# Kernel optimization log

Hardware: AMD Instinct MI355X
Metric: run time of the kernel (lower is better)

The kernel has to match this reference:

```python
import jax, jax.numpy as jnp
import numpy as np

TOP_K = 8
ROUTED_SCALING_FACTOR = 2.5
NORM_TOPK_PROB = True


def setup_inputs() -> dict:
    key = jax.random.key(0)
    k1, k2 = jax.random.split(key)
    hidden_states = jax.random.normal(k1, (4, 4096, 4096), dtype=jnp.float32)
    # gate weight: (n_routed_experts, hidden_size)
    weight = jax.random.normal(k2, (256, 4096), dtype=jnp.float32) * (1.0 / np.sqrt(4096))
    return {"hidden_states": hidden_states, "weight": weight}


def reference(hidden_states, weight):
    bsz, seq_len, h = hidden_states.shape
    x = hidden_states.reshape(-1, h).astype(jnp.float32)  # [T, h]
    # gate logits: [T, E]
    logits = jnp.einsum("th,eh->te", x, weight.astype(jnp.float32))
    scores = jax.nn.softmax(logits, axis=-1)
    topk_weight, topk_idx = jax.lax.top_k(scores, TOP_K)  # [T, k]
    if TOP_K > 1 and NORM_TOPK_PROB:
        denom = jnp.sum(topk_weight, axis=-1, keepdims=True) + 1e-20
        topk_weight = topk_weight / denom * ROUTED_SCALING_FACTOR
    else:
        topk_weight = topk_weight * ROUTED_SCALING_FACTOR
    return (topk_idx, topk_weight)
```

## Files before the change

kernel.cpp:

```cpp
#include <hip/hip_runtime.h>
#include <math.h>

typedef _Float16 half8  __attribute__((ext_vector_type(8)));
typedef _Float16 half4v __attribute__((ext_vector_type(4)));
typedef float    f32x16 __attribute__((ext_vector_type(16)));

namespace {
constexpr int H      = 4096;
constexpr int E      = 256;
constexpr int TOPK   = 8;
constexpr int NCAND  = 12;
constexpr int BM     = 64;
constexpr int BK     = 32;
constexpr int NCHUNK = H / BK;
constexpr int SLD    = E + 4;
constexpr float DELTA = 5e-4f;
constexpr size_t WF_BYTES = (size_t)E * H * 2 * 2;
constexpr int SMEM_BYTES = BM * SLD * 4;
}

__global__ void convert_w_kernel(const float* __restrict__ W,
                                 _Float16* __restrict__ Wf) {
    int t  = blockIdx.x * blockDim.x + threadIdx.x;
    int e  = t >> 10;
    int kq = t & 1023;
    float4 w4 = *(const float4*)(W + ((size_t)e << 12) + (kq << 2));
    float x0 = w4.x * 64.0f, x1 = w4.y * 64.0f, x2 = w4.z * 64.0f, x3 = w4.w * 64.0f;
    _Float16 h0 = (_Float16)x0, h1 = (_Float16)x1, h2 = (_Float16)x2, h3 = (_Float16)x3;
    _Float16 l0 = (_Float16)(x0 - (float)h0), l1 = (_Float16)(x1 - (float)h1);
    _Float16 l2 = (_Float16)(x2 - (float)h2), l3 = (_Float16)(x3 - (float)h3);
    int k    = kq << 2;
    int nt   = e >> 5;
    int ks   = k >> 4;
    int lane = (e & 31) | (((k >> 3) & 1) << 5);
    int j    = k & 7;
    size_t base = (((size_t)nt * 256 + ks) * 2) * 512 + lane * 8 + j;
    half4v hv = {h0, h1, h2, h3};
    half4v lv = {l0, l1, l2, l3};
    *(half4v*)(Wf + base)       = hv;
    *(half4v*)(Wf + base + 512) = lv;
}

struct BF { half8 h[2][2]; half8 l[2][2]; };

__global__ __launch_bounds__(512, 2)
void moe_gate_mfma(const float* __restrict__ X, const _Float16* __restrict__ Wf,
                   const float* __restrict__ Wg,
                   float* __restrict__ out_idx, float* __restrict__ out_w) {
    __shared__ __align__(16) char smem[SMEM_BYTES];
    _Float16* Abuf = (_Float16*)smem;
    float*    sc   = (float*)smem;

    const int tid  = threadIdx.x;
    const int lane = tid & 63;
    const int wave = tid >> 6;
    const int wr   = wave >> 2;
    const int wc   = wave & 3;
    const int m0   = blockIdx.x * BM;

    const int m_s  = tid >> 3;
    const int kq_s = tid & 7;
    const int ks_s = kq_s >> 2;
    const int mt_s = m_s >> 5;
    const int ln_s = (m_s & 31) | (((kq_s >> 1) & 1) << 5);
    const int j_s  = (kq_s & 1) * 4;
    const int dst_s = ((ks_s * 2 + mt_s) * 2) * 512 + ln_s * 8 + j_s;
    const float* xgp = X + (size_t)(m0 + m_s) * H + kq_s * 4;

    f32x16 acc[2];
    #pragma unroll
    for (int nt = 0; nt < 2; ++nt)
        #pragma unroll
        for (int r = 0; r < 16; ++r) acc[nt][r] = 0.0f;

    auto load_b = [&](int kc, BF& b) {
        #pragma unroll
        for (int ks = 0; ks < 2; ++ks)
            #pragma unroll
            for (int nt = 0; nt < 2; ++nt) {
                size_t base = (((size_t)(2 * wc + nt) * 256 + (kc * 2 + ks)) * 2) * 512
                              + lane * 8;
                b.h[ks][nt] = *(const half8*)(Wf + base);
                b.l[ks][nt] = *(const half8*)(Wf + base + 512);
            }
    };
    auto stage = [&](int bufIdx, float4 xv) {
        _Float16* buf = Abuf + bufIdx * 4096;
        float x0 = xv.x, x1 = xv.y, x2 = xv.z, x3 = xv.w;
        _Float16 h0 = (_Float16)x0, h1 = (_Float16)x1, h2 = (_Float16)x2, h3 = (_Float16)x3;
        _Float16 l0 = (_Float16)(x0 - (float)h0), l1 = (_Float16)(x1 - (float)h1);
        _Float16 l2 = (_Float16)(x2 - (float)h2), l3 = (_Float16)(x3 - (float)h3);
        half4v hv = {h0, h1, h2, h3};
        half4v lv = {l0, l1, l2, l3};
        *(half4v*)(buf + dst_s)       = hv;
        *(half4v*)(buf + dst_s + 512) = lv;
    };
    auto compute = [&](int bufIdx, const BF& b) {
        const _Float16* buf = Abuf + bufIdx * 4096;
        #pragma unroll
        for (int ks = 0; ks < 2; ++ks) {
            const _Float16* p = buf + (ks * 2 + wr) * 1024 + lane * 8;
            half8 a_hi = *(const half8*)p;
            half8 a_lo = *(const half8*)(p + 512);
            #pragma unroll
            for (int nt = 0; nt < 2; ++nt) {
                acc[nt] = __builtin_amdgcn_mfma_f32_32x32x16_f16(a_hi, b.h[ks][nt], acc[nt], 0, 0, 0);
                acc[nt] = __builtin_amdgcn_mfma_f32_32x32x16_f16(a_lo, b.h[ks][nt], acc[nt], 0, 0, 0);
                acc[nt] = __builtin_amdgcn_mfma_f32_32x32x16_f16(a_hi, b.l[ks][nt], acc[nt], 0, 0, 0);
            }
        }
    };

    BF bcur;
    load_b(0, bcur);
    float4 xv = *(const float4*)(xgp);
    stage(0, xv);
    __syncthreads();
    float4 xnxt = *(const float4*)(xgp + BK);

    for (int kc = 0; kc < NCHUNK; ++kc) {
        BF bnxt;
        float4 xfar = make_float4(0.f, 0.f, 0.f, 0.f);
        if (kc + 1 < NCHUNK) load_b(kc + 1, bnxt);
        if (kc + 2 < NCHUNK) xfar = *(const float4*)(xgp + (size_t)(kc + 2) * BK);
        compute(kc & 1, bcur);
        if (kc + 1 < NCHUNK) {
            stage((kc + 1) & 1, xnxt);
            __syncthreads();
        }
        bcur = bnxt;
        xnxt = xfar;
    }

    __syncthreads();
    #pragma unroll
    for (int nt = 0; nt < 2; ++nt) {
        #pragma unroll
        for (int r = 0; r < 16; ++r) {
            int row = (r & 3) + 8 * (r >> 2) + 4 * (lane >> 5);
            int col = lane & 31;
            sc[(wr * 32 + row) * SLD + wc * 64 + nt * 32 + col] = acc[nt][r] * 0.015625f;
        }
    }
    __syncthreads();

    for (int t8 = 0; t8 < 8; ++t8) {
        const int t = wave * 8 + t8;
        float4 pv = *(const float4*)(sc + t * SLD + lane * 4);
        float p0 = pv.x, p1 = pv.y, p2 = pv.z, p3 = pv.w;

        float tv[NCAND]; int ti[NCAND];
        #pragma unroll
        for (int s = 0; s < NCAND; ++s) {
            float bv = p0; int bi = lane * 4;
            if (p1 > bv || (p1 == bv && lane * 4 + 1 < bi)) { bv = p1; bi = lane * 4 + 1; }
            if (p2 > bv || (p2 == bv && lane * 4 + 2 < bi)) { bv = p2; bi = lane * 4 + 2; }
            if (p3 > bv || (p3 == bv && lane * 4 + 3 < bi)) { bv = p3; bi = lane * 4 + 3; }
            #pragma unroll
            for (int off = 32; off > 0; off >>= 1) {
                float ov = __shfl_xor(bv, off, 64);
                int   oi = __shfl_xor(bi, off, 64);
                if (ov > bv || (ov == bv && oi < bi)) { bv = ov; bi = oi; }
            }
            tv[s] = bv; ti[s] = bi;
            if ((bi >> 2) == lane) {
                const int sl = bi & 3;
                if      (sl == 0) p0 = -3e38f;
                else if (sl == 1) p1 = -3e38f;
                else if (sl == 2) p2 = -3e38f;
                else              p3 = -3e38f;
            }
        }

        bool rescue = false;
        #pragma unroll
        for (int g = 0; g < 9; ++g) rescue |= (tv[g] - tv[g + 1] < DELTA);

        if (rescue) {
            double dv[NCAND];
            const float* xr = X + (size_t)(m0 + t) * H;
            #pragma unroll 1
            for (int c = 0; c < NCAND; ++c) {
                const float* wrow = Wg + (size_t)ti[c] * H;
                double s_ = 0.0;
                #pragma unroll
                for (int it = 0; it < 16; ++it) {
                    float4 xa = *(const float4*)(xr + it * 256 + lane * 4);
                    float4 wa = *(const float4*)(wrow + it * 256 + lane * 4);
                    s_ += (double)xa.x * wa.x + (double)xa.y * wa.y
                        + (double)xa.z * wa.z + (double)xa.w * wa.w;
                }
                #pragma unroll
                for (int off = 32; off > 0; off >>= 1) s_ += __shfl_xor(s_, off, 64);
                dv[c] = s_;
            }
            int si[NCAND];
            #pragma unroll
            for (int c = 0; c < NCAND; ++c) si[c] = ti[c];
            #pragma unroll
            for (int a = 0; a < TOPK; ++a) {
                int best = a;
                #pragma unroll
                for (int b = a + 1; b < NCAND; ++b) {
                    if (dv[b] > dv[best] || (dv[b] == dv[best] && si[b] < si[best])) best = b;
                }
                double tdv = dv[a]; dv[a] = dv[best]; dv[best] = tdv;
                int    tsi = si[a]; si[a] = si[best]; si[best] = tsi;
            }
            #pragma unroll
            for (int s = 0; s < TOPK; ++s) { tv[s] = (float)dv[s]; ti[s] = si[s]; }
        }

        if (lane == 0) {
            float M = tv[0];
            float e8[TOPK]; float den = 0.0f;
            #pragma unroll
            for (int s = 0; s < TOPK; ++s) { e8[s] = expf(tv[s] - M); den += e8[s]; }
            float scl = 2.5f / den;
            size_t tok = (size_t)(m0 + t);
            #pragma unroll
            for (int s = 0; s < TOPK; ++s) {
                out_idx[tok * TOPK + s] = (float)ti[s];
                out_w[tok * TOPK + s]   = e8[s] * scl;
            }
        }
    }
}

namespace fb {
constexpr int BM = 32, BK = 32;
constexpr int XS_LD = BM + 4, WS_LD = E + 4;
constexpr int LDS_FLOATS = BK * XS_LD + BK * WS_LD;
}

__global__ __launch_bounds__(256, 2)
void moe_gate_fallback(const float* __restrict__ X, const float* __restrict__ W,
                       float* __restrict__ out_idx, float* __restrict__ out_w) {
    __shared__ float lds[fb::LDS_FLOATS];
    float* xs = lds;
    float* ws = lds + fb::BK * fb::XS_LD;
    const int tid = threadIdx.x;
    const int tx = tid & 31, ty = tid >> 5;
    const int m0 = blockIdx.x * fb::BM;
    float acc[4][8];
    #pragma unroll
    for (int i = 0; i < 4; ++i)
        #pragma unroll
        for (int j = 0; j < 8; ++j) acc[i][j] = 0.0f;
    const int lr = tid >> 3, lc = (tid & 7) * 4;
    const float* xg = X + (size_t)(m0 + lr) * H + lc;
    const float* wg = W + (size_t)lr * H + lc;
    for (int kc = 0; kc < H; kc += fb::BK) {
        float4 xv = *(const float4*)(xg + kc);
        float4 wv[8];
        #pragma unroll
        for (int i = 0; i < 8; ++i) wv[i] = *(const float4*)(wg + (size_t)i * 32 * H + kc);
        __syncthreads();
        #pragma unroll
        for (int j = 0; j < 4; ++j) xs[(lc + j) * fb::XS_LD + lr] = ((const float*)&xv)[j];
        #pragma unroll
        for (int i = 0; i < 8; ++i)
            #pragma unroll
            for (int j = 0; j < 4; ++j)
                ws[(lc + j) * fb::WS_LD + i * 32 + lr] = ((const float*)&wv[i])[j];
        __syncthreads();
        #pragma unroll
        for (int kk = 0; kk < fb::BK; ++kk) {
            float4 xa = *(const float4*)(xs + kk * fb::XS_LD + ty * 4);
            float4 wb0 = *(const float4*)(ws + kk * fb::WS_LD + tx * 8);
            float4 wb1 = *(const float4*)(ws + kk * fb::WS_LD + tx * 8 + 4);
            const float xr[4] = {xa.x, xa.y, xa.z, xa.w};
            const float wr8[8] = {wb0.x, wb0.y, wb0.z, wb0.w, wb1.x, wb1.y, wb1.z, wb1.w};
            #pragma unroll
            for (int i = 0; i < 4; ++i)
                #pragma unroll
                for (int j = 0; j < 8; ++j) acc[i][j] = fmaf(xr[i], wr8[j], acc[i][j]);
        }
    }
    __syncthreads();
    float* sc = lds;
    #pragma unroll
    for (int i = 0; i < 4; ++i) {
        *(float4*)(sc + (ty * 4 + i) * fb::WS_LD + tx * 8) =
            make_float4(acc[i][0], acc[i][1], acc[i][2], acc[i][3]);
        *(float4*)(sc + (ty * 4 + i) * fb::WS_LD + tx * 8 + 4) =
            make_float4(acc[i][4], acc[i][5], acc[i][6], acc[i][7]);
    }
    __syncthreads();
    const int wave = tid >> 6, lane = tid & 63;
    for (int t8 = 0; t8 < 8; ++t8) {
        const int t = wave * 8 + t8;
        float4 pv = *(const float4*)(sc + t * fb::WS_LD + lane * 4);
        float v0 = pv.x, v1 = pv.y, v2 = pv.z, v3 = pv.w;
        float M = fmaxf(fmaxf(v0, v1), fmaxf(v2, v3));
        #pragma unroll
        for (int off = 32; off > 0; off >>= 1) M = fmaxf(M, __shfl_xor(M, off, 64));
        float p0 = expf(v0 - M), p1 = expf(v1 - M), p2 = expf(v2 - M), p3 = expf(v3 - M);
        float z = p0 + p1 + p2 + p3;
        #pragma unroll
        for (int off = 32; off > 0; off >>= 1) z += __shfl_xor(z, off, 64);
        p0 /= z; p1 /= z; p2 /= z; p3 /= z;
        float tv[TOPK]; int ti[TOPK];
        #pragma unroll
        for (int s = 0; s < TOPK; ++s) {
            float bv = p0; int bi = lane * 4;
            if (p1 > bv || (p1 == bv && lane * 4 + 1 < bi)) { bv = p1; bi = lane * 4 + 1; }
            if (p2 > bv || (p2 == bv && lane * 4 + 2 < bi)) { bv = p2; bi = lane * 4 + 2; }
            if (p3 > bv || (p3 == bv && lane * 4 + 3 < bi)) { bv = p3; bi = lane * 4 + 3; }
            #pragma unroll
            for (int off = 32; off > 0; off >>= 1) {
                float ov = __shfl_xor(bv, off, 64);
                int   oi = __shfl_xor(bi, off, 64);
                if (ov > bv || (ov == bv && oi < bi)) { bv = ov; bi = oi; }
            }
            tv[s] = bv; ti[s] = bi;
            if ((bi >> 2) == lane) {
                const int sl = bi & 3;
                if      (sl == 0) p0 = -1.0f;
                else if (sl == 1) p1 = -1.0f;
                else if (sl == 2) p2 = -1.0f;
                else              p3 = -1.0f;
            }
        }
        if (lane == 0) {
            float den = tv[0] + tv[1] + tv[2] + tv[3] + tv[4] + tv[5] + tv[6] + tv[7] + 1e-20f;
            float scl = 2.5f / den;
            size_t tok = (size_t)(m0 + t);
            #pragma unroll
            for (int s = 0; s < TOPK; ++s) {
                out_idx[tok * TOPK + s] = (float)ti[s];
                out_w[tok * TOPK + s]   = tv[s] * scl;
            }
        }
    }
}

extern "C" void kernel_launch(void* const* d_in, const int* in_sizes, int n_in,
                              void* d_out, int out_size, void* d_ws, size_t ws_size,
                              hipStream_t stream) {
    const float* X = (const float*)d_in[0];
    const float* W = (const float*)d_in[1];
    float* out = (float*)d_out;
    const int T = in_sizes[0] / H;
    float* out_idx = out;
    float* out_w   = out + (size_t)T * TOPK;

    if (ws_size >= WF_BYTES && (T % BM) == 0) {
        _Float16* Wf = (_Float16*)d_ws;
        hipLaunchKernelGGL(convert_w_kernel, dim3((E * (H / 4)) / 256), dim3(256), 0, stream, W, Wf);
        hipLaunchKernelGGL(moe_gate_mfma, dim3(T / BM), dim3(512), 0, stream, X, Wf, W, out_idx, out_w);
    } else {
        hipLaunchKernelGGL(moe_gate_fallback, dim3(T / fb::BM), dim3(256), 0, stream, X, W, out_idx, out_w);
    }
}
```

Before: 686.4 us.

## Load X fragments directly into registers, dropping LDS staging and barriers

Each wave now reads its own A fragments from global memory straight into registers and does the fp16 hi/lo split in registers. This replaces the shared-memory staging buffer and the per-chunk __syncthreads. The goal is to remove the LDS round trip and the block-wide barrier on every K chunk. In exchange, each X row is read redundantly by the 4 column-waves, which quadruples global and L2 traffic for X, and the hi/lo conversion work is duplicated across those waves. Register pressure also rises from the double-buffered float4 fragments.

```diff
diff --git a/kernel.cpp b/kernel.cpp
--- a/kernel.cpp
+++ b/kernel.cpp
@@ -11,12 +11,10 @@
 constexpr int TOPK   = 8;
 constexpr int NCAND  = 12;
 constexpr int BM     = 64;
-constexpr int BK     = 32;
-constexpr int NCHUNK = H / BK;
+constexpr int NCHUNK = H / 32;
 constexpr int SLD    = E + 4;
 constexpr float DELTA = 5e-4f;
 constexpr size_t WF_BYTES = (size_t)E * H * 2 * 2;
-constexpr int SMEM_BYTES = BM * SLD * 4;
 }
 
 __global__ void convert_w_kernel(const float* __restrict__ W,
@@ -41,15 +39,11 @@
     *(half4v*)(Wf + base + 512) = lv;
 }
 
-struct BF { half8 h[2][2]; half8 l[2][2]; };
-
 __global__ __launch_bounds__(512, 2)
 void moe_gate_mfma(const float* __restrict__ X, const _Float16* __restrict__ Wf,
                    const float* __restrict__ Wg,
                    float* __restrict__ out_idx, float* __restrict__ out_w) {
-    __shared__ __align__(16) char smem[SMEM_BYTES];
-    _Float16* Abuf = (_Float16*)smem;
-    float*    sc   = (float*)smem;
+    __shared__ float sc[BM * SLD];
 
     const int tid  = threadIdx.x;
     const int lane = tid & 63;
@@ -58,14 +52,8 @@
     const int wc   = wave & 3;
     const int m0   = blockIdx.x * BM;
 
-    const int m_s  = tid >> 3;
-    const int kq_s = tid & 7;
-    const int ks_s = kq_s >> 2;
-    const int mt_s = m_s >> 5;
-    const int ln_s = (m_s & 31) | (((kq_s >> 1) & 1) << 5);
-    const int j_s  = (kq_s & 1) * 4;
-    const int dst_s = ((ks_s * 2 + mt_s) * 2) * 512 + ln_s * 8 + j_s;
-    const float* xgp = X + (size_t)(m0 + m_s) * H + kq_s * 4;
+    const float*    ap = X + (size_t)(m0 + wr * 32 + (lane & 31)) * H + ((lane >> 5) * 8);
+    const _Float16* bp = Wf + lane * 8;
 
     f32x16 acc[2];
     #pragma unroll
@@ -73,66 +61,59 @@
         #pragma unroll
         for (int r = 0; r < 16; ++r) acc[nt][r] = 0.0f;
 
-    auto load_b = [&](int kc, BF& b) {
+    float4 af[2][2][2];
+    half8  bh[2][2][2], bl[2][2][2];
+
+    auto load_a = [&](int kc, int buf) {
+        #pragma unroll
+        for (int ks = 0; ks < 2; ++ks) {
+            const float* p = ap + kc * 32 + ks * 16;
+            af[buf][ks][0] = *(const float4*)(p);
+            af[buf][ks][1] = *(const float4*)(p + 4);
+        }
+    };
+    auto load_bf = [&](int kc, int buf) {
         #pragma unroll
         for (int ks = 0; ks < 2; ++ks)
             #pragma unroll
             for (int nt = 0; nt < 2; ++nt) {
-                size_t base = (((size_t)(2 * wc + nt) * 256 + (kc * 2 + ks)) * 2) * 512
-                              + lane * 8;
-                b.h[ks][nt] = *(const half8*)(Wf + base);
-                b.l[ks][nt] = *(const half8*)(Wf + base + 512);
+                const _Float16* p = bp
+                    + (((size_t)(2 * wc + nt) * 256 + (kc * 2 + ks)) * 2) * 512;
+                bh[buf][ks][nt] = *(const half8*)(p);
+                bl[buf][ks][nt] = *(const half8*)(p + 512);
             }
     };
-    auto stage = [&](int bufIdx, float4 xv) {
-        _Float16* buf = Abuf + bufIdx * 4096;
-        float x0 = xv.x, x1 = xv.y, x2 = xv.z, x3 = xv.w;
-        _Float16 h0 = (_Float16)x0, h1 = (_Float16)x1, h2 = (_Float16)x2, h3 = (_Float16)x3;
-        _Float16 l0 = (_Float16)(x0 - (float)h0), l1 = (_Float16)(x1 - (float)h1);
-        _Float16 l2 = (_Float16)(x2 - (float)h2), l3 = (_Float16)(x3 - (float)h3);
-        half4v hv = {h0, h1, h2, h3};
-        half4v lv = {l0, l1, l2, l3};
-        *(half4v*)(buf + dst_s)       = hv;
-        *(half4v*)(buf + dst_s + 512) = lv;
-    };
-    auto compute = [&](int bufIdx, const BF& b) {
-        const _Float16* buf = Abuf + bufIdx * 4096;
+
+    load_a(0, 0);
+    load_bf(0, 0);
+
+    #pragma unroll 2
+    for (int kc = 0; kc < NCHUNK; ++kc) {
+        const int cur = kc & 1, nxt = cur ^ 1;
+        const int kn  = (kc + 1 < NCHUNK) ? kc + 1 : kc;
+        load_a(kn, nxt);
+        load_bf(kn, nxt);
         #pragma unroll
         for (int ks = 0; ks < 2; ++ks) {
-            const _Float16* p = buf + (ks * 2 + wr) * 1024 + lane * 8;
-            half8 a_hi = *(const half8*)p;
-            half8 a_lo = *(const half8*)(p + 512);
+            float xr[8];
+            *(float4*)&xr[0] = af[cur][ks][0];
+            *(float4*)&xr[4] = af[cur][ks][1];
+            half8 a_hi, a_lo;
+            #pragma unroll
+            for (int j = 0; j < 8; ++j) {
+                _Float16 h = (_Float16)xr[j];
+                a_hi[j] = h;
+                a_lo[j] = (_Float16)(xr[j] - (float)h);
+            }
             #pragma unroll
             for (int nt = 0; nt < 2; ++nt) {
-                acc[nt] = __builtin_amdgcn_mfma_f32_32x32x16_f16(a_hi, b.h[ks][nt], acc[nt], 0, 0, 0);
-                acc[nt] = __builtin_amdgcn_mfma_f32_32x32x16_f16(a_lo, b.h[ks][nt], acc[nt], 0, 0, 0);
-                acc[nt] = __builtin_amdgcn_mfma_f32_32x32x16_f16(a_hi, b.l[ks][nt], acc[nt], 0, 0, 0);
-            }
-        }
-    };
-
-    BF bcur;
-    load_b(0, bcur);
-    float4 xv = *(const float4*)(xgp);
-    stage(0, xv);
-    __syncthreads();
-    float4 xnxt = *(const float4*)(xgp + BK);
-
-    for (int kc = 0; kc < NCHUNK; ++kc) {
-        BF bnxt;
-        float4 xfar = make_float4(0.f, 0.f, 0.f, 0.f);
-        if (kc + 1 < NCHUNK) load_b(kc + 1, bnxt);
-        if (kc + 2 < NCHUNK) xfar = *(const float4*)(xgp + (size_t)(kc + 2) * BK);
-        compute(kc & 1, bcur);
-        if (kc + 1 < NCHUNK) {
-            stage((kc + 1) & 1, xnxt);
-            __syncthreads();
-        }
-        bcur = bnxt;
-        xnxt = xfar;
-    }
-
-    __syncthreads();
+                acc[nt] = __builtin_amdgcn_mfma_f32_32x32x16_f16(a_hi, bh[cur][ks][nt], acc[nt], 0, 0, 0);
+                acc[nt] = __builtin_amdgcn_mfma_f32_32x32x16_f16(a_lo, bh[cur][ks][nt], acc[nt], 0, 0, 0);
+                acc[nt] = __builtin_amdgcn_mfma_f32_32x32x16_f16(a_hi, bl[cur][ks][nt], acc[nt], 0, 0, 0);
+            }
+        }
+    }
+
     #pragma unroll
     for (int nt = 0; nt < 2; ++nt) {
         #pragma unroll
```

After: 734.5 us. +7.0%, slower.
